# Kernel tuning notes

Hardware: AMD Instinct MI355X
Metric: run time of the kernel (lower is better)

The kernel has to match this reference:

```python
import jax, jax.numpy as jnp
import numpy as np
import math

D, H, HKV = 1024, 16, 4
DH = D // H  # 64
B, T = 2, 2048


def _rope_tables(T, Dh):
    pos = jnp.arange(T, dtype=jnp.float32)
    inv_freq = 1.0 / (10000.0 ** (jnp.arange(0, Dh, 2, dtype=jnp.float32) / Dh))
    ang = pos[:, None] * inv_freq[None, :]                 # [T, Dh/2]
    ang = jnp.concatenate([ang, ang], axis=-1)             # [T, Dh]
    return jnp.cos(ang)[None, None], jnp.sin(ang)[None, None]  # [1,1,T,Dh]


def setup_inputs() -> dict:
    key = jax.random.key(0)
    kx, kq, kk, kv, ko = jax.random.split(key, 5)
    x = jax.random.normal(kx, (B, T, D), dtype=jnp.float32)
    s = 1.0 / math.sqrt(D)
    Wq = jax.random.normal(kq, (H * DH, D), dtype=jnp.float32) * s
    Wk = jax.random.normal(kk, (HKV * DH, D), dtype=jnp.float32) * s
    Wv = jax.random.normal(kv, (HKV * DH, D), dtype=jnp.float32) * s
    Wo = jax.random.normal(ko, (D, D), dtype=jnp.float32) * s
    rope_cos, rope_sin = _rope_tables(T, DH)
    # additive causal mask: 0 on/below diagonal, -1e9 above
    causal = jnp.triu(jnp.full((T, T), -1e9, dtype=jnp.float32), k=1)[None, None]
    return {"x": x, "rope_cos": rope_cos, "rope_sin": rope_sin,
            "attn_mask": causal, "Wq": Wq, "Wk": Wk, "Wv": Wv, "Wo": Wo}


def _apply_rope(t, cos, sin):
    # t: [B,h,T,Dh]; cos/sin broadcast [1,1,T,Dh]
    Dh = t.shape[-1]
    t1, t2 = t[..., :Dh // 2], t[..., Dh // 2:]
    t_rot = jnp.concatenate([-t2, t1], axis=-1)
    Tlen = t.shape[2]
    return t * cos[..., :Tlen, :] + t_rot * sin[..., :Tlen, :]


def reference(x, rope_cos, rope_sin, attn_mask, Wq, Wk, Wv, Wo):
    Bx, Tx, Dx = x.shape
    q = (x @ Wq.T).reshape(Bx, Tx, H, DH).transpose(0, 2, 1, 3)    # [B,H,T,Dh]
    k = (x @ Wk.T).reshape(Bx, Tx, HKV, DH).transpose(0, 2, 1, 3)  # [B,Hkv,T,Dh]
    v = (x @ Wv.T).reshape(Bx, Tx, HKV, DH).transpose(0, 2, 1, 3)
    q = _apply_rope(q, rope_cos, rope_sin)
    k = _apply_rope(k, rope_cos, rope_sin)
    rep = H // HKV
    k = jnp.repeat(k, rep, axis=1)  # repeat_interleave on head dim
    v = jnp.repeat(v, rep, axis=1)
    att = jnp.einsum('bhtd,bhsd->bhts', q, k) / math.sqrt(DH)
    att = att + attn_mask
    att = jax.nn.softmax(att, axis=-1)
    y = jnp.einsum('bhts,bhsd->bhtd', att, v)
    y = y.transpose(0, 2, 1, 3).reshape(Bx, Tx, Dx)
    return y @ Wo.T
```

## Files before the change

### kernel.cpp

```cpp
#include <hip/hip_runtime.h>


typedef short bf16x8 __attribute__((ext_vector_type(8)));
typedef float f32x4 __attribute__((ext_vector_type(4)));

__device__ __forceinline__ unsigned short f2bf(float f) {
  unsigned u = __float_as_uint(f);
  u += 0x7fffu + ((u >> 16) & 1u);
  return (unsigned short)(u >> 16);
}

__device__ __forceinline__ unsigned cvt_pk_bf16(float lo, float hi) {
  unsigned r;
  asm("v_cvt_pk_bf16_f32 %0, %1, %2" : "=v"(r) : "v"(lo), "v"(hi));
  return r;
}

__device__ __forceinline__ float fexp2(float x) {
#if __has_builtin(__builtin_amdgcn_exp2f)
  return __builtin_amdgcn_exp2f(x);
#else
  return __expf(x * 0.69314718056f);
#endif
}

__device__ __forceinline__ void load_lds16(const void* g, void* l) {
  __builtin_amdgcn_global_load_lds(
      (const __attribute__((address_space(1))) void*)g,
      (__attribute__((address_space(3))) void*)l, 16, 0, 0);
}

__global__ __launch_bounds__(256) void cvt_kernel(const float* __restrict__ src,
                                                  unsigned short* __restrict__ dst,
                                                  int n4) {
  int i = blockIdx.x * blockDim.x + threadIdx.x;
  if (i >= n4) return;
  float4 v = reinterpret_cast<const float4*>(src)[i];
  ushort4 o;
  o.x = f2bf(v.x); o.y = f2bf(v.y); o.z = f2bf(v.z); o.w = f2bf(v.w);
  reinterpret_cast<ushort4*>(dst)[i] = o;
}

__global__ __launch_bounds__(256) void cvt_w4(const float* __restrict__ Wq,
                                              const float* __restrict__ Wk,
                                              const float* __restrict__ Wv,
                                              const float* __restrict__ Wo,
                                              unsigned short* __restrict__ Wcat,
                                              unsigned short* __restrict__ Wob) {
  int i = blockIdx.x * blockDim.x + threadIdx.x;
  const float* src; unsigned short* dst; int off;
  if (i < 262144)      { src = Wq; dst = Wcat;           off = i; }
  else if (i < 327680) { src = Wk; dst = Wcat + 1048576; off = i - 262144; }
  else if (i < 393216) { src = Wv; dst = Wcat + 1310720; off = i - 327680; }
  else                 { src = Wo; dst = Wob;            off = i - 393216; }
  float4 v = reinterpret_cast<const float4*>(src)[off];
  ushort4 o;
  o.x = f2bf(v.x); o.y = f2bf(v.y); o.z = f2bf(v.z); o.w = f2bf(v.w);
  reinterpret_cast<ushort4*>(dst)[off] = o;
}

__global__ __launch_bounds__(256) void gemm_bt(const unsigned short* __restrict__ A,
                                               const unsigned short* __restrict__ B,
                                               float* __restrict__ C,
                                               int M, int N, int K) {
  __shared__ unsigned short As[2][128][32];
  __shared__ unsigned short Bs[2][128][32];
  const int tid  = threadIdx.x;
  const int lane = tid & 63, wave = tid >> 6;
  const int wr = wave >> 1, wc = wave & 1;
  const int m0 = blockIdx.y * 128, n0 = blockIdx.x * 128;
  const int fr = lane & 15, k8 = (lane >> 4) * 8;
  const int nT = K >> 5;
  f32x4 acc[4][4] = {};

  const int scs0 = wave, scs1 = 4 + wave;
#define GSTAGE(sel, kt)                                                          \
  {                                                                              \
    {                                                                            \
      const int c = scs0*64 + lane, row = c >> 2, col = (c & 3) * 8;             \
      load_lds16(A + (size_t)(m0 + row)*K + (kt) + col,                          \
                 (char*)&As[sel][0][0] + (size_t)scs0*1024);                     \
      load_lds16(B + (size_t)(n0 + row)*K + (kt) + col,                          \
                 (char*)&Bs[sel][0][0] + (size_t)scs0*1024);                     \
    }                                                                            \
    {                                                                            \
      const int c = scs1*64 + lane, row = c >> 2, col = (c & 3) * 8;             \
      load_lds16(A + (size_t)(m0 + row)*K + (kt) + col,                          \
                 (char*)&As[sel][0][0] + (size_t)scs1*1024);                     \
      load_lds16(B + (size_t)(n0 + row)*K + (kt) + col,                          \
                 (char*)&Bs[sel][0][0] + (size_t)scs1*1024);                     \
    }                                                                            \
  }

  GSTAGE(0, 0);
  __syncthreads();
  for (int t = 0; t < nT; ++t) {
    const int cur = t & 1;
    if (t + 1 < nT) GSTAGE(cur ^ 1, (t + 1) * 32);
    bf16x8 af[4], bf[4];
#pragma unroll
    for (int i = 0; i < 4; ++i) af[i] = *(const bf16x8*)&As[cur][wr*64 + i*16 + fr][k8];
#pragma unroll
    for (int i = 0; i < 4; ++i) bf[i] = *(const bf16x8*)&Bs[cur][wc*64 + i*16 + fr][k8];
#pragma unroll
    for (int mi = 0; mi < 4; ++mi)
#pragma unroll
      for (int ni = 0; ni < 4; ++ni)
        acc[mi][ni] = __builtin_amdgcn_mfma_f32_16x16x32_bf16(af[mi], bf[ni], acc[mi][ni], 0, 0, 0);
    __syncthreads();
  }
#pragma unroll
  for (int mi = 0; mi < 4; ++mi)
#pragma unroll
    for (int ni = 0; ni < 4; ++ni)
#pragma unroll
      for (int j = 0; j < 4; ++j) {
        int row = m0 + wr*64 + mi*16 + (lane >> 4)*4 + j;
        int col = n0 + wc*64 + ni*16 + fr;
        C[(size_t)row * N + col] = acc[mi][ni][j];
      }
}

__global__ __launch_bounds__(256) void gemm_qkv_rope(const unsigned short* __restrict__ A,
                                                     const unsigned short* __restrict__ Bw,
                                                     const float* __restrict__ rc,
                                                     const float* __restrict__ rs,
                                                     unsigned short* __restrict__ Qb,
                                                     unsigned short* __restrict__ Kb,
                                                     unsigned short* __restrict__ Vb) {
  const int K = 1024;
  __shared__ unsigned short As[2][128][32];
  __shared__ unsigned short Bs[2][128][32];
  const int tid  = threadIdx.x;
  const int lane = tid & 63, wave = tid >> 6;
  const int wr = wave >> 1, wc = wave & 1;
  const int m0 = blockIdx.y * 128, n0 = blockIdx.x * 128;
  const int fr = lane & 15, k8 = (lane >> 4) * 8;
  f32x4 acc[4][4] = {};
  const int scs0 = wave, scs1 = 4 + wave;
#define QSTAGE(sel, kt)                                                          \
  {                                                                              \
    {                                                                            \
      const int c = scs0*64 + lane, row = c >> 2, col = (c & 3) * 8;             \
      load_lds16(A  + (size_t)(m0 + row)*K + (kt) + col,                         \
                 (char*)&As[sel][0][0] + (size_t)scs0*1024);                     \
      load_lds16(Bw + (size_t)(n0 + row)*K + (kt) + col,                         \
                 (char*)&Bs[sel][0][0] + (size_t)scs0*1024);                     \
    }                                                                            \
    {                                                                            \
      const int c = scs1*64 + lane, row = c >> 2, col = (c & 3) * 8;             \
      load_lds16(A  + (size_t)(m0 + row)*K + (kt) + col,                         \
                 (char*)&As[sel][0][0] + (size_t)scs1*1024);                     \
      load_lds16(Bw + (size_t)(n0 + row)*K + (kt) + col,                         \
                 (char*)&Bs[sel][0][0] + (size_t)scs1*1024);                     \
    }                                                                            \
  }
  QSTAGE(0, 0);
  __syncthreads();
  for (int t = 0; t < 32; ++t) {
    const int cur = t & 1;
    if (t + 1 < 32) QSTAGE(cur ^ 1, (t + 1) * 32);
    bf16x8 af[4], bf[4];
#pragma unroll
    for (int i = 0; i < 4; ++i) af[i] = *(const bf16x8*)&As[cur][wr*64 + i*16 + fr][k8];
#pragma unroll
    for (int i = 0; i < 4; ++i) bf[i] = *(const bf16x8*)&Bs[cur][wc*64 + i*16 + fr][k8];
#pragma unroll
    for (int mi = 0; mi < 4; ++mi)
#pragma unroll
      for (int ni = 0; ni < 4; ++ni)
        acc[mi][ni] = __builtin_amdgcn_mfma_f32_16x16x32_bf16(af[mi], bf[ni], acc[mi][ni], 0, 0, 0);
    __syncthreads();
  }
  const int rg = lane >> 4;
  const float SCLQ = 0.125f * 1.44269504089f;
  const int colbase = n0 + wc*64;
#pragma unroll
  for (int mi = 0; mi < 4; ++mi) {
#pragma unroll
    for (int j = 0; j < 4; ++j) {
      const int m = m0 + wr*64 + mi*16 + rg*4 + j;
      const int b = m >> 11, t = m & 2047;
      if (colbase < 1280) {
        float vr[4];
#pragma unroll
        for (int ni = 0; ni < 4; ++ni) {
          const int d = ni*16 + fr;
          float cs = rc[t*64 + d], sn = rs[t*64 + d];
          float x = acc[mi][ni][j];
          float partner = acc[mi][ni ^ 2][j];
          float rot = (ni < 2) ? -partner : partner;
          vr[ni] = x * cs + rot * sn;
        }
        if (colbase < 1024) {
          const int h = colbase >> 6;
          size_t base = ((size_t)((b*16 + h)*2048 + t) << 6);
#pragma unroll
          for (int ni = 0; ni < 4; ++ni) Qb[base + ni*16 + fr] = f2bf(vr[ni] * SCLQ);
        } else {
          const int kh = (colbase - 1024) >> 6;
          size_t base = ((size_t)((b*4 + kh)*2048 + t) << 6);
#pragma unroll
          for (int ni = 0; ni < 4; ++ni) Kb[base + ni*16 + fr] = f2bf(vr[ni]);
        }
      } else {
        const int vh = (colbase - 1280) >> 6;
#pragma unroll
        for (int ni = 0; ni < 4; ++ni) {
          const int d = ni*16 + fr;
          Vb[((size_t)((b*4 + vh)*64 + d))*2048 + t] = f2bf(acc[mi][ni][j]);
        }
      }
    }
  }
}

__global__ __launch_bounds__(256) void attn_kernel(const unsigned short* __restrict__ Qb,
                                                   const unsigned short* __restrict__ Kb,
                                                   const unsigned short* __restrict__ Vb,
                                                   unsigned short* __restrict__ Yb) {
  __shared__ unsigned short Ks[2][64][72];
  __shared__ unsigned short Vt[2][64][72];
  __shared__ unsigned PpA[4][32][20];
  __shared__ unsigned PpB[4][32][20];
  const int p = blockIdx.x, bh = blockIdx.y;
  const int b = bh >> 4, h = bh & 15, kvh = h >> 2;
  const int qtA = 31 - p, qtB = p;
  const int nkv = qtA + 1;
  const int tid = threadIdx.x;
  const int wave = tid >> 6, lane = tid & 63;
  const int fr = lane & 15, g = lane >> 4, k8 = g * 8;
  const int srow = tid >> 3, scol = (tid & 7) * 8;
  const unsigned short* Kp = Kb + ((size_t)(b*4 + kvh)*2048) * 64;
  const unsigned short* Vp = Vb + ((size_t)(b*4 + kvh)*64) * 2048;
  const unsigned short* QpA = Qb + ((size_t)((b*16 + h)*2048 + qtA*64)) * 64;
  const unsigned short* QpB = Qb + ((size_t)((b*16 + h)*2048 + qtB*64)) * 64;
  bf16x8 qfA0 = *(const bf16x8*)(QpA + (wave*16 + fr)*64 + k8);
  bf16x8 qfA1 = *(const bf16x8*)(QpA + (wave*16 + fr)*64 + 32 + k8);
  bf16x8 qfB0 = *(const bf16x8*)(QpB + (wave*16 + fr)*64 + k8);
  bf16x8 qfB1 = *(const bf16x8*)(QpB + (wave*16 + fr)*64 + 32 + k8);
  float mA = -3.0e38f, lsA = 0.f, mB = -3.0e38f, lsB = 0.f;
  f32x4 accA[4] = {}, accB[4] = {};
  const int qgA = qtA*64 + wave*16 + fr;
  const int qgB = qtB*64 + wave*16 + fr;

  bf16x8 kreg[2], vreg[2];
#pragma unroll
  for (int j = 0; j < 2; ++j) {
    kreg[j] = *(const bf16x8*)(Kp + (size_t)(srow + j*32)*64 + scol);
    vreg[j] = *(const bf16x8*)(Vp + (size_t)(srow + j*32)*2048 + scol);
  }
#pragma unroll
  for (int j = 0; j < 2; ++j) {
    *(bf16x8*)&Ks[0][srow + j*32][scol] = kreg[j];
    *(bf16x8*)&Vt[0][srow + j*32][scol] = vreg[j];
  }
  __syncthreads();

  for (int kt = 0; kt < nkv; ++kt) {
    const int kv0 = kt * 64;
    const int cur = kt & 1;
    const bool actB = (kt <= qtB);
    const bool more = (kt + 1 < nkv);
    if (more) {
      const size_t nv0 = (size_t)(kt + 1) * 64;
#pragma unroll
      for (int j = 0; j < 2; ++j) {
        kreg[j] = *(const bf16x8*)(Kp + (nv0 + srow + j*32)*64 + scol);
        vreg[j] = *(const bf16x8*)(Vp + (size_t)(srow + j*32)*2048 + nv0 + scol);
      }
    }
    f32x4 sA[4] = {}, sB[4] = {};
    __builtin_amdgcn_s_setprio(1);
#pragma unroll
    for (int n = 0; n < 4; ++n) {
      bf16x8 kf0 = *(const bf16x8*)&Ks[cur][n*16 + fr][k8];
      sA[n] = __builtin_amdgcn_mfma_f32_16x16x32_bf16(kf0, qfA0, sA[n], 0, 0, 0);
      if (actB) sB[n] = __builtin_amdgcn_mfma_f32_16x16x32_bf16(kf0, qfB0, sB[n], 0, 0, 0);
      bf16x8 kf1 = *(const bf16x8*)&Ks[cur][n*16 + fr][32 + k8];
      sA[n] = __builtin_amdgcn_mfma_f32_16x16x32_bf16(kf1, qfA1, sA[n], 0, 0, 0);
      if (actB) sB[n] = __builtin_amdgcn_mfma_f32_16x16x32_bf16(kf1, qfB1, sB[n], 0, 0, 0);
    }
    __builtin_amdgcn_s_setprio(0);
    {
      float sv[4][4];
      if (kt == qtA) {
#pragma unroll
        for (int n = 0; n < 4; ++n)
#pragma unroll
          for (int r = 0; r < 4; ++r)
            sv[n][r] = (kv0 + n*16 + g*4 + r > qgA) ? -3.0e38f : sA[n][r];
      } else {
#pragma unroll
        for (int n = 0; n < 4; ++n)
#pragma unroll
          for (int r = 0; r < 4; ++r) sv[n][r] = sA[n][r];
      }
      float t4[4];
#pragma unroll
      for (int n = 0; n < 4; ++n)
        t4[n] = fmaxf(fmaxf(sv[n][0], sv[n][1]), fmaxf(sv[n][2], sv[n][3]));
      float tm = fmaxf(fmaxf(t4[0], t4[1]), fmaxf(t4[2], t4[3]));
      tm = fmaxf(tm, __shfl_xor(tm, 16));
      tm = fmaxf(tm, __shfl_xor(tm, 32));
      float mn = fmaxf(mA, tm);
      float al = fexp2(mA - mn);
      mA = mn;
      lsA *= al;
#pragma unroll
      for (int dt = 0; dt < 4; ++dt) accA[dt] *= al;
#pragma unroll
      for (int n = 0; n < 4; ++n)
#pragma unroll
        for (int r2 = 0; r2 < 2; ++r2) {
          float p0 = fexp2(sv[n][2*r2]   - mA);
          float p1 = fexp2(sv[n][2*r2+1] - mA);
          lsA += p0 + p1;
          PpA[wave][n*8 + g*2 + r2][fr] = cvt_pk_bf16(p0, p1);
        }
    }
    if (actB) {
      float sv[4][4];
      if (kt == qtB) {
#pragma unroll
        for (int n = 0; n < 4; ++n)
#pragma unroll
          for (int r = 0; r < 4; ++r)
            sv[n][r] = (kv0 + n*16 + g*4 + r > qgB) ? -3.0e38f : sB[n][r];
      } else {
#pragma unroll
        for (int n = 0; n < 4; ++n)
#pragma unroll
          for (int r = 0; r < 4; ++r) sv[n][r] = sB[n][r];
      }
      float t4[4];
#pragma unroll
      for (int n = 0; n < 4; ++n)
        t4[n] = fmaxf(fmaxf(sv[n][0], sv[n][1]), fmaxf(sv[n][2], sv[n][3]));
      float tm = fmaxf(fmaxf(t4[0], t4[1]), fmaxf(t4[2], t4[3]));
      tm = fmaxf(tm, __shfl_xor(tm, 16));
      tm = fmaxf(tm, __shfl_xor(tm, 32));
      float mn = fmaxf(mB, tm);
      float al = fexp2(mB - mn);
      mB = mn;
      lsB *= al;
#pragma unroll
      for (int dt = 0; dt < 4; ++dt) accB[dt] *= al;
#pragma unroll
      for (int n = 0; n < 4; ++n)
#pragma unroll
        for (int r2 = 0; r2 < 2; ++r2) {
          float p0 = fexp2(sv[n][2*r2]   - mB);
          float p1 = fexp2(sv[n][2*r2+1] - mB);
          lsB += p0 + p1;
          PpB[wave][n*8 + g*2 + r2][fr] = cvt_pk_bf16(p0, p1);
        }
    }
    __builtin_amdgcn_s_setprio(1);
#pragma unroll
    for (int c = 0; c < 2; ++c) {
      union { unsigned u[4]; bf16x8 v; } pa, pb;
#pragma unroll
      for (int i2 = 0; i2 < 4; ++i2) pa.u[i2] = PpA[wave][c*16 + g*4 + i2][fr];
      if (actB) {
#pragma unroll
        for (int i2 = 0; i2 < 4; ++i2) pb.u[i2] = PpB[wave][c*16 + g*4 + i2][fr];
      }
#pragma unroll
      for (int dt = 0; dt < 4; ++dt) {
        bf16x8 vf = *(const bf16x8*)&Vt[cur][dt*16 + fr][c*32 + k8];
        accA[dt] = __builtin_amdgcn_mfma_f32_16x16x32_bf16(vf, pa.v, accA[dt], 0, 0, 0);
        if (actB) accB[dt] = __builtin_amdgcn_mfma_f32_16x16x32_bf16(vf, pb.v, accB[dt], 0, 0, 0);
      }
    }
    __builtin_amdgcn_s_setprio(0);
    if (more) {
#pragma unroll
      for (int j = 0; j < 2; ++j) {
        *(bf16x8*)&Ks[cur ^ 1][srow + j*32][scol] = kreg[j];
        *(bf16x8*)&Vt[cur ^ 1][srow + j*32][scol] = vreg[j];
      }
      __syncthreads();
    }
  }
  {
    float ls = lsA;
    ls += __shfl_xor(ls, 16);
    ls += __shfl_xor(ls, 32);
    const float inv = 1.0f / ls;
    size_t base = ((size_t)(b*2048 + qgA) << 10) + h*64;
#pragma unroll
    for (int dt = 0; dt < 4; ++dt) {
      uint2 pk;
      pk.x = cvt_pk_bf16(accA[dt][0] * inv, accA[dt][1] * inv);
      pk.y = cvt_pk_bf16(accA[dt][2] * inv, accA[dt][3] * inv);
      *(uint2*)&Yb[base + dt*16 + g*4] = pk;
    }
  }
  {
    float ls = lsB;
    ls += __shfl_xor(ls, 16);
    ls += __shfl_xor(ls, 32);
    const float inv = 1.0f / ls;
    size_t base = ((size_t)(b*2048 + qgB) << 10) + h*64;
#pragma unroll
    for (int dt = 0; dt < 4; ++dt) {
      uint2 pk;
      pk.x = cvt_pk_bf16(accB[dt][0] * inv, accB[dt][1] * inv);
      pk.y = cvt_pk_bf16(accB[dt][2] * inv, accB[dt][3] * inv);
      *(uint2*)&Yb[base + dt*16 + g*4] = pk;
    }
  }
}

extern "C" void kernel_launch(void* const* d_in, const int* in_sizes, int n_in,
                              void* d_out, int out_size, void* d_ws, size_t ws_size,
                              hipStream_t stream) {
  const float* x  = (const float*)d_in[0];
  const float* rc = (const float*)d_in[1];
  const float* rs = (const float*)d_in[2];
  const float* Wq = (const float*)d_in[4];
  const float* Wk = (const float*)d_in[5];
  const float* Wv = (const float*)d_in[6];
  const float* Wo = (const float*)d_in[7];
  float* out = (float*)d_out;

  char* ws = (char*)d_ws;
  unsigned short* xb   = (unsigned short*)(ws);
  unsigned short* Wcat = (unsigned short*)(ws + 8388608);
  unsigned short* Wob  = (unsigned short*)(ws + 11534336);
  unsigned short* Qb   = (unsigned short*)(ws + 38797312);
  unsigned short* Kb   = (unsigned short*)(ws + 47185920);
  unsigned short* Vb   = (unsigned short*)(ws + 49283072);
  unsigned short* Yb   = (unsigned short*)(ws + 51380224);

  cvt_kernel<<<4096, 256, 0, stream>>>(x, xb, 1048576);
  cvt_w4<<<2560, 256, 0, stream>>>(Wq, Wk, Wv, Wo, Wcat, Wob);
  gemm_qkv_rope<<<dim3(12, 32), 256, 0, stream>>>(xb, Wcat, rc, rs, Qb, Kb, Vb);
  attn_kernel<<<dim3(16, 32), 256, 0, stream>>>(Qb, Kb, Vb, Yb);
  gemm_bt<<<dim3(8, 32), 256, 0, stream>>>(Yb, Wob, out, 4096, 1024, 1024);
}
```

Measured before the change: 134.8 us.

## Split paired causal query tiles into one query tile per attention block

```diff
diff --git a/kernel.cpp b/kernel.cpp
--- a/kernel.cpp
+++ b/kernel.cpp
@@ -72,7 +72,6 @@
   const int fr = lane & 15, k8 = (lane >> 4) * 8;
   const int nT = K >> 5;
   f32x4 acc[4][4] = {};
-
   const int scs0 = wave, scs1 = 4 + wave;
 #define GSTAGE(sel, kt)                                                          \
   {                                                                              \
@@ -91,7 +90,6 @@
                  (char*)&Bs[sel][0][0] + (size_t)scs1*1024);                     \
     }                                                                            \
   }
-
   GSTAGE(0, 0);
   __syncthreads();
   for (int t = 0; t < nT; ++t) {
@@ -221,28 +219,22 @@
                                                    unsigned short* __restrict__ Yb) {
   __shared__ unsigned short Ks[2][64][72];
   __shared__ unsigned short Vt[2][64][72];
-  __shared__ unsigned PpA[4][32][20];
-  __shared__ unsigned PpB[4][32][20];
-  const int p = blockIdx.x, bh = blockIdx.y;
+  __shared__ unsigned Pp[4][32][20];
+  const int qt = 31 - blockIdx.x, bh = blockIdx.y;
   const int b = bh >> 4, h = bh & 15, kvh = h >> 2;
-  const int qtA = 31 - p, qtB = p;
-  const int nkv = qtA + 1;
+  const int nkv = qt + 1;
   const int tid = threadIdx.x;
   const int wave = tid >> 6, lane = tid & 63;
   const int fr = lane & 15, g = lane >> 4, k8 = g * 8;
   const int srow = tid >> 3, scol = (tid & 7) * 8;
   const unsigned short* Kp = Kb + ((size_t)(b*4 + kvh)*2048) * 64;
   const unsigned short* Vp = Vb + ((size_t)(b*4 + kvh)*64) * 2048;
-  const unsigned short* QpA = Qb + ((size_t)((b*16 + h)*2048 + qtA*64)) * 64;
-  const unsigned short* QpB = Qb + ((size_t)((b*16 + h)*2048 + qtB*64)) * 64;
-  bf16x8 qfA0 = *(const bf16x8*)(QpA + (wave*16 + fr)*64 + k8);
-  bf16x8 qfA1 = *(const bf16x8*)(QpA + (wave*16 + fr)*64 + 32 + k8);
-  bf16x8 qfB0 = *(const bf16x8*)(QpB + (wave*16 + fr)*64 + k8);
-  bf16x8 qfB1 = *(const bf16x8*)(QpB + (wave*16 + fr)*64 + 32 + k8);
-  float mA = -3.0e38f, lsA = 0.f, mB = -3.0e38f, lsB = 0.f;
-  f32x4 accA[4] = {}, accB[4] = {};
-  const int qgA = qtA*64 + wave*16 + fr;
-  const int qgB = qtB*64 + wave*16 + fr;
+  const unsigned short* Qp = Qb + ((size_t)((b*16 + h)*2048 + qt*64)) * 64;
+  bf16x8 qf0 = *(const bf16x8*)(Qp + (wave*16 + fr)*64 + k8);
+  bf16x8 qf1 = *(const bf16x8*)(Qp + (wave*16 + fr)*64 + 32 + k8);
+  float m = -3.0e38f, ls = 0.f;
+  f32x4 acc[4] = {};
+  const int qg = qt*64 + wave*16 + fr;
 
   bf16x8 kreg[2], vreg[2];
 #pragma unroll
@@ -260,7 +252,6 @@
   for (int kt = 0; kt < nkv; ++kt) {
     const int kv0 = kt * 64;
     const int cur = kt & 1;
-    const bool actB = (kt <= qtB);
     const bool more = (kt + 1 < nkv);
     if (more) {
       const size_t nv0 = (size_t)(kt + 1) * 64;
@@ -270,31 +261,29 @@
         vreg[j] = *(const bf16x8*)(Vp + (size_t)(srow + j*32)*2048 + nv0 + scol);
       }
     }
-    f32x4 sA[4] = {}, sB[4] = {};
+    f32x4 s[4] = {};
     __builtin_amdgcn_s_setprio(1);
 #pragma unroll
     for (int n = 0; n < 4; ++n) {
       bf16x8 kf0 = *(const bf16x8*)&Ks[cur][n*16 + fr][k8];
-      sA[n] = __builtin_amdgcn_mfma_f32_16x16x32_bf16(kf0, qfA0, sA[n], 0, 0, 0);
-      if (actB) sB[n] = __builtin_amdgcn_mfma_f32_16x16x32_bf16(kf0, qfB0, sB[n], 0, 0, 0);
+      s[n] = __builtin_amdgcn_mfma_f32_16x16x32_bf16(kf0, qf0, s[n], 0, 0, 0);
       bf16x8 kf1 = *(const bf16x8*)&Ks[cur][n*16 + fr][32 + k8];
-      sA[n] = __builtin_amdgcn_mfma_f32_16x16x32_bf16(kf1, qfA1, sA[n], 0, 0, 0);
-      if (actB) sB[n] = __builtin_amdgcn_mfma_f32_16x16x32_bf16(kf1, qfB1, sB[n], 0, 0, 0);
+      s[n] = __builtin_amdgcn_mfma_f32_16x16x32_bf16(kf1, qf1, s[n], 0, 0, 0);
     }
     __builtin_amdgcn_s_setprio(0);
     {
       float sv[4][4];
-      if (kt == qtA) {
+      if (kt == qt) {
 #pragma unroll
         for (int n = 0; n < 4; ++n)
 #pragma unroll
           for (int r = 0; r < 4; ++r)
-            sv[n][r] = (kv0 + n*16 + g*4 + r > qgA) ? -3.0e38f : sA[n][r];
+            sv[n][r] = (kv0 + n*16 + g*4 + r > qg) ? -3.0e38f : s[n][r];
       } else {
 #pragma unroll
         for (int n = 0; n < 4; ++n)
 #pragma unroll
-          for (int r = 0; r < 4; ++r) sv[n][r] = sA[n][r];
+          for (int r = 0; r < 4; ++r) sv[n][r] = s[n][r];
       }
       float t4[4];
 #pragma unroll
@@ -303,74 +292,32 @@
       float tm = fmaxf(fmaxf(t4[0], t4[1]), fmaxf(t4[2], t4[3]));
       tm = fmaxf(tm, __shfl_xor(tm, 16));
       tm = fmaxf(tm, __shfl_xor(tm, 32));
-      float mn = fmaxf(mA, tm);
-      float al = fexp2(mA - mn);
-      mA = mn;
-      lsA *= al;
-#pragma unroll
-      for (int dt = 0; dt < 4; ++dt) accA[dt] *= al;
+      float mn = fmaxf(m, tm);
+      float al = fexp2(m - mn);
+      m = mn;
+      ls *= al;
+#pragma unroll
+      for (int dt = 0; dt < 4; ++dt) acc[dt] *= al;
 #pragma unroll
       for (int n = 0; n < 4; ++n)
 #pragma unroll
         for (int r2 = 0; r2 < 2; ++r2) {
-          float p0 = fexp2(sv[n][2*r2]   - mA);
-          float p1 = fexp2(sv[n][2*r2+1] - mA);
-          lsA += p0 + p1;
-          PpA[wave][n*8 + g*2 + r2][fr] = cvt_pk_bf16(p0, p1);
+          float p0 = fexp2(sv[n][2*r2]   - m);
+          float p1 = fexp2(sv[n][2*r2+1] - m);
+          ls += p0 + p1;
+          Pp[wave][n*8 + g*2 + r2][fr] = cvt_pk_bf16(p0, p1);
         }
     }
-    if (actB) {
-      float sv[4][4];
-      if (kt == qtB) {
-#pragma unroll
-        for (int n = 0; n < 4; ++n)
-#pragma unroll
-          for (int r = 0; r < 4; ++r)
-            sv[n][r] = (kv0 + n*16 + g*4 + r > qgB) ? -3.0e38f : sB[n][r];
-      } else {
-#pragma unroll
-        for (int n = 0; n < 4; ++n)
-#pragma unroll
-          for (int r = 0; r < 4; ++r) sv[n][r] = sB[n][r];
-      }
-      float t4[4];
-#pragma unroll
-      for (int n = 0; n < 4; ++n)
-        t4[n] = fmaxf(fmaxf(sv[n][0], sv[n][1]), fmaxf(sv[n][2], sv[n][3]));
-      float tm = fmaxf(fmaxf(t4[0], t4[1]), fmaxf(t4[2], t4[3]));
-      tm = fmaxf(tm, __shfl_xor(tm, 16));
-      tm = fmaxf(tm, __shfl_xor(tm, 32));
-      float mn = fmaxf(mB, tm);
-      float al = fexp2(mB - mn);
-      mB = mn;
-      lsB *= al;
-#pragma unroll
-      for (int dt = 0; dt < 4; ++dt) accB[dt] *= al;
-#pragma unroll
-      for (int n = 0; n < 4; ++n)
-#pragma unroll
-        for (int r2 = 0; r2 < 2; ++r2) {
-          float p0 = fexp2(sv[n][2*r2]   - mB);
-          float p1 = fexp2(sv[n][2*r2+1] - mB);
-          lsB += p0 + p1;
-          PpB[wave][n*8 + g*2 + r2][fr] = cvt_pk_bf16(p0, p1);
-        }
-    }
     __builtin_amdgcn_s_setprio(1);
 #pragma unroll
     for (int c = 0; c < 2; ++c) {
-      union { unsigned u[4]; bf16x8 v; } pa, pb;
-#pragma unroll
-      for (int i2 = 0; i2 < 4; ++i2) pa.u[i2] = PpA[wave][c*16 + g*4 + i2][fr];
-      if (actB) {
-#pragma unroll
-        for (int i2 = 0; i2 < 4; ++i2) pb.u[i2] = PpB[wave][c*16 + g*4 + i2][fr];
-      }
+      union { unsigned u[4]; bf16x8 v; } pa;
+#pragma unroll
+      for (int i2 = 0; i2 < 4; ++i2) pa.u[i2] = Pp[wave][c*16 + g*4 + i2][fr];
 #pragma unroll
       for (int dt = 0; dt < 4; ++dt) {
         bf16x8 vf = *(const bf16x8*)&Vt[cur][dt*16 + fr][c*32 + k8];
-        accA[dt] = __builtin_amdgcn_mfma_f32_16x16x32_bf16(vf, pa.v, accA[dt], 0, 0, 0);
-        if (actB) accB[dt] = __builtin_amdgcn_mfma_f32_16x16x32_bf16(vf, pb.v, accB[dt], 0, 0, 0);
+        acc[dt] = __builtin_amdgcn_mfma_f32_16x16x32_bf16(vf, pa.v, acc[dt], 0, 0, 0);
       }
     }
     __builtin_amdgcn_s_setprio(0);
@@ -384,30 +331,16 @@
     }
   }
   {
-    float ls = lsA;
-    ls += __shfl_xor(ls, 16);
-    ls += __shfl_xor(ls, 32);
-    const float inv = 1.0f / ls;
-    size_t base = ((size_t)(b*2048 + qgA) << 10) + h*64;
+    float lsr = ls;
+    lsr += __shfl_xor(lsr, 16);
+    lsr += __shfl_xor(lsr, 32);
+    const float inv = 1.0f / lsr;
+    size_t base = ((size_t)(b*2048 + qg) << 10) + h*64;
 #pragma unroll
     for (int dt = 0; dt < 4; ++dt) {
       uint2 pk;
-      pk.x = cvt_pk_bf16(accA[dt][0] * inv, accA[dt][1] * inv);
-      pk.y = cvt_pk_bf16(accA[dt][2] * inv, accA[dt][3] * inv);
-      *(uint2*)&Yb[base + dt*16 + g*4] = pk;
-    }
-  }
-  {
-    float ls = lsB;
-    ls += __shfl_xor(ls, 16);
-    ls += __shfl_xor(ls, 32);
-    const float inv = 1.0f / ls;
-    size_t base = ((size_t)(b*2048 + qgB) << 10) + h*64;
-#pragma unroll
-    for (int dt = 0; dt < 4; ++dt) {
-      uint2 pk;
-      pk.x = cvt_pk_bf16(accB[dt][0] * inv, accB[dt][1] * inv);
-      pk.y = cvt_pk_bf16(accB[dt][2] * inv, accB[dt][3] * inv);
+      pk.x = cvt_pk_bf16(acc[dt][0] * inv, acc[dt][1] * inv);
+      pk.y = cvt_pk_bf16(acc[dt][2] * inv, acc[dt][3] * inv);
       *(uint2*)&Yb[base + dt*16 + g*4] = pk;
     }
   }
@@ -437,6 +370,6 @@
   cvt_kernel<<<4096, 256, 0, stream>>>(x, xb, 1048576);
   cvt_w4<<<2560, 256, 0, stream>>>(Wq, Wk, Wv, Wo, Wcat, Wob);
   gemm_qkv_rope<<<dim3(12, 32), 256, 0, stream>>>(xb, Wcat, rc, rs, Qb, Kb, Vb);
-  attn_kernel<<<dim3(16, 32), 256, 0, stream>>>(Qb, Kb, Vb, Yb);
+  attn_kernel<<<dim3(32, 32), 256, 0, stream>>>(Qb, Kb, Vb, Yb);
   gemm_bt<<<dim3(8, 32), 256, 0, stream>>>(Yb, Wob, out, 4096, 1024, 1024);
 }
```

After: 163.0 us. 1.21x slower.
